# Kernel tuning notes

Measured on AMD Instinct MI355X. Metric: run time of the kernel, lower is better.

The kernel has to match this reference:

```python
import jax, jax.numpy as jnp
import numpy as np

HIDDEN = 16  # hk.LSTM(16)


def lstm_scan(x, W, b, reverse):
    """Haiku LSTM unroll. x: [B,T,D]; W: [D+H, 4H]; b: [4H]. Returns [B,T,H]."""
    B = x.shape[0]

    def step(carry, xt):
        h, c = carry
        gated = jnp.concatenate([xt, h], axis=-1) @ W + b
        i, g, f, o = jnp.split(gated, 4, axis=-1)
        f = jax.nn.sigmoid(f + 1.0)  # haiku forget-gate bias of +1
        c = f * c + jax.nn.sigmoid(i) * jnp.tanh(g)
        h = jax.nn.sigmoid(o) * jnp.tanh(c)
        return (h, c), h

    init = (jnp.zeros((B, HIDDEN), x.dtype), jnp.zeros((B, HIDDEN), x.dtype))
    xt = jnp.swapaxes(x, 0, 1)  # [T,B,D] time-major for scan
    _, outs = jax.lax.scan(step, init, xt, reverse=reverse)
    return jnp.swapaxes(outs, 0, 1)  # [B,T,H]


def setup_inputs() -> dict:
    key = jax.random.key(0)
    ks = jax.random.split(key, 8)
    B, T, D = 4096, 256, 20
    E, H, M, OUT = 64, HIDDEN, 16, 2

    def glorot(k, shape):
        fan_in = shape[0]
        return (jax.random.normal(k, shape, jnp.float32) / np.sqrt(fan_in)).astype(jnp.float32)

    return {
        "x": jax.random.normal(ks[0], (B, T, D), jnp.float32),
        "W0": glorot(ks[1], (D, E)), "b0": jnp.zeros((E,), jnp.float32),
        "Wf": glorot(ks[2], (E + H, 4 * H)), "bf": jnp.zeros((4 * H,), jnp.float32),
        "Wb": glorot(ks[3], (E + H, 4 * H)), "bb": jnp.zeros((4 * H,), jnp.float32),
        "W1": glorot(ks[4], (2 * H, E)), "b1": jnp.zeros((E,), jnp.float32),
        "W2": glorot(ks[5], (E, M)), "b2": jnp.zeros((M,), jnp.float32),
        "W3": glorot(ks[6], (M, OUT)), "b3": jnp.zeros((OUT,), jnp.float32),
    }


def reference(x, W0, b0, Wf, bf, Wb, bb, W1, b1, W2, b2, W3, b3):
    h = jax.nn.relu(x @ W0 + b0)                 # [B,T,64]
    fwd = lstm_scan(h, Wf, bf, reverse=False)    # [B,T,16]
    bwd = lstm_scan(h, Wb, bb, reverse=True)     # [B,T,16], output[t] uses future state
    outs = jnp.concatenate([fwd, bwd], axis=-1)[:, -1, :]  # take last time step, [B,32]
    outs = jax.nn.relu(outs @ W1 + b1)
    outs = jax.nn.relu(outs @ W2 + b2)
    return outs @ W3 + b3
```

## Files before the change

kernel.cpp:

```cpp
#include <hip/hip_runtime.h>


typedef __attribute__((ext_vector_type(8))) short short8;
typedef __attribute__((ext_vector_type(4))) float floatx4;

union F8 { uint32_t u[4]; short8 v; };
union H2 { uint32_t u; _Float16 h[2]; };
union B8 { uint4 q[2]; uint32_t d[8]; };

#define LDW  66
#define LDW2 68

#define LOG2E 1.44269504088896340736f

__device__ __forceinline__ float tanh_fast(float x) {
    float e = __expf(-2.f * x);
    return __fdividef(2.f, 1.f + e) - 1.f;
}

#define ROT(v, S) __int_as_float(__builtin_amdgcn_mov_dpp(__float_as_int(v), 0x120 | (S), 0xf, 0xf, false))

__device__ __forceinline__ void split_pack(const float* f, uint32_t* hi, uint32_t* lo) {
#pragma unroll
    for (int i = 0; i < 4; ++i) {
        uint32_t u0 = __float_as_uint(f[2 * i]), u1 = __float_as_uint(f[2 * i + 1]);
        hi[i] = __builtin_amdgcn_perm(u1, u0, 0x07060302u);
        float r0 = f[2 * i]     - __uint_as_float(u0 & 0xFFFF0000u);
        float r1 = f[2 * i + 1] - __uint_as_float(u1 & 0xFFFF0000u);
        lo[i] = __builtin_amdgcn_perm(__float_as_uint(r1), __float_as_uint(r0), 0x07060302u);
    }
}

__global__ __launch_bounds__(256, 2)
void gpre_gemm(const float* __restrict__ x,
               const float* __restrict__ W0, const float* __restrict__ b0,
               const float* __restrict__ Wf, const float* __restrict__ bf,
               uint32_t* __restrict__ gph)
{
    __shared__ __align__(16) float tA[4][16 * LDW2];
    __shared__ __align__(16) float tB[4][16 * LDW2];

    const int tid  = threadIdx.x;
    const int wv   = tid >> 6;
    const int j    = tid & 63;
    const int nl   = j & 15;
    const int quad = j >> 4;

    F8 B1h[4], B1l[4];
#pragma unroll
    for (int T = 0; T < 4; ++T) {
        float w[8];
#pragma unroll
        for (int e = 0; e < 8; ++e) {
            int k = quad * 8 + e;
            w[e] = (k < 20) ? W0[k * 64 + T * 16 + nl] : 0.f;
        }
        split_pack(w, B1h[T].u, B1l[T].u);
    }
    F8 B2h[4][2], B2l[4][2];
#pragma unroll
    for (int T = 0; T < 4; ++T) {
        const float sgT = (T == 1) ? (-2.f * LOG2E) : (-LOG2E);
#pragma unroll
        for (int KH = 0; KH < 2; ++KH) {
            float w[8];
#pragma unroll
            for (int e = 0; e < 8; ++e) {
                int k = KH * 32 + quad * 8 + e;
                w[e] = Wf[k * 64 + T * 16 + nl] * sgT;
            }
            split_pack(w, B2h[T][KH].u, B2l[T][KH].u);
        }
    }

    float b0v[4], bfv[4];
#pragma unroll
    for (int T = 0; T < 4; ++T) {
        const float sgT = (T == 1) ? (-2.f * LOG2E) : (-LOG2E);
        b0v[T] = b0[T * 16 + nl];
        bfv[T] = (bf[T * 16 + nl] + ((T == 2) ? 1.f : 0.f)) * sgT;
    }

    const size_t base = (size_t)(blockIdx.x * 4 + wv) * 256;

    float4 xp0, xp1;
    {
        const float* xr = x + (base + nl) * 20;
        if (quad < 2) {
            xp0 = *(const float4*)(xr + quad * 8);
            xp1 = *(const float4*)(xr + quad * 8 + 4);
        } else if (quad == 2) {
            xp0 = *(const float4*)(xr + 16);
            xp1 = (float4){0.f, 0.f, 0.f, 0.f};
        } else {
            xp0 = (float4){0.f, 0.f, 0.f, 0.f};
            xp1 = (float4){0.f, 0.f, 0.f, 0.f};
        }
    }

#pragma unroll 1
    for (int tile = 0; tile < 16; ++tile) {
        float xk[8] = {xp0.x, xp0.y, xp0.z, xp0.w, xp1.x, xp1.y, xp1.z, xp1.w};

        {
            int tn = (tile < 15) ? (tile + 1) : 15;
            const float* xr = x + (base + tn * 16 + nl) * 20;
            if (quad < 2) {
                xp0 = *(const float4*)(xr + quad * 8);
                xp1 = *(const float4*)(xr + quad * 8 + 4);
            } else if (quad == 2) {
                xp0 = *(const float4*)(xr + 16);
            }
        }

        F8 A1h, A1l;
        split_pack(xk, A1h.u, A1l.u);

        floatx4 acc1[4];
#pragma unroll
        for (int T = 0; T < 4; ++T) acc1[T] = (floatx4){b0v[T], b0v[T], b0v[T], b0v[T]};
#pragma unroll
        for (int T = 0; T < 4; ++T) {
            acc1[T] = __builtin_amdgcn_mfma_f32_16x16x32_bf16(A1h.v, B1h[T].v, acc1[T], 0, 0, 0);
            acc1[T] = __builtin_amdgcn_mfma_f32_16x16x32_bf16(A1l.v, B1h[T].v, acc1[T], 0, 0, 0);
            acc1[T] = __builtin_amdgcn_mfma_f32_16x16x32_bf16(A1h.v, B1l[T].v, acc1[T], 0, 0, 0);
        }

#pragma unroll
        for (int T = 0; T < 4; ++T)
#pragma unroll
            for (int reg = 0; reg < 4; ++reg)
                tA[wv][(quad * 4 + reg) * LDW2 + T * 16 + nl] = fmaxf(acc1[T][reg], 0.f);
        __builtin_amdgcn_wave_barrier();

        F8 A2h[2], A2l[2];
#pragma unroll
        for (int KH = 0; KH < 2; ++KH) {
            float xe[8];
#pragma unroll
            for (int e = 0; e < 8; ++e)
                xe[e] = tA[wv][nl * LDW2 + KH * 32 + quad * 8 + e];
            split_pack(xe, A2h[KH].u, A2l[KH].u);
        }

        floatx4 acc2[4];
#pragma unroll
        for (int T = 0; T < 4; ++T) acc2[T] = (floatx4){bfv[T], bfv[T], bfv[T], bfv[T]};
#pragma unroll
        for (int T = 0; T < 4; ++T)
#pragma unroll
            for (int KH = 0; KH < 2; ++KH) {
                acc2[T] = __builtin_amdgcn_mfma_f32_16x16x32_bf16(A2h[KH].v, B2h[T][KH].v, acc2[T], 0, 0, 0);
                acc2[T] = __builtin_amdgcn_mfma_f32_16x16x32_bf16(A2l[KH].v, B2h[T][KH].v, acc2[T], 0, 0, 0);
                acc2[T] = __builtin_amdgcn_mfma_f32_16x16x32_bf16(A2h[KH].v, B2l[T][KH].v, acc2[T], 0, 0, 0);
            }

#pragma unroll
        for (int T = 0; T < 4; ++T)
#pragma unroll
            for (int reg = 0; reg < 4; ++reg)
                tB[wv][(quad * 4 + reg) * LDW2 + T * 16 + nl] = acc2[T][reg];
        __builtin_amdgcn_wave_barrier();

        {
            B8 r;
#pragma unroll
            for (int tp = 0; tp < 8; ++tp) {
                float a0 = tB[wv][(2 * tp) * LDW2 + j];
                float a1 = tB[wv][(2 * tp + 1) * LDW2 + j];
                H2 pk;
                pk.h[0] = (_Float16)a0;
                pk.h[1] = (_Float16)a1;
                r.d[tp] = pk.u;
            }
            uint32_t* gp = gph + ((size_t)(blockIdx.x * 4 + wv) * 16 + tile) * 512 + j * 8;
            *(uint4*)(gp)     = r.q[0];
            *(uint4*)(gp + 4) = r.q[1];
        }
        __builtin_amdgcn_wave_barrier();
    }
}

__global__ __launch_bounds__(256, 4)
void lstm_scan(const uint32_t* __restrict__ gph,
               const float* __restrict__ x,
               const float* __restrict__ W0, const float* __restrict__ b0,
               const float* __restrict__ Wf,
               const float* __restrict__ Wb, const float* __restrict__ bb,
               const float* __restrict__ W1, const float* __restrict__ b1,
               const float* __restrict__ W2, const float* __restrict__ b2,
               const float* __restrict__ W3, const float* __restrict__ b3,
               float* __restrict__ out)
{
    __shared__ __align__(16) float xh_sh[4][64];
    __shared__ __align__(16) float h_sh[4][48];

    const int wv   = threadIdx.x >> 6;
    const int j    = threadIdx.x & 63;
    const int b    = blockIdx.x * 4 + wv;
    const int nl   = j & 15;
    const int quad = j >> 4;

    int rot1 = __builtin_amdgcn_mov_dpp(j, 0x121, 0xf, 0xf, false);
    const bool plus = ((rot1 & 15) == ((nl + 1) & 15));

    const float sj = (quad == 1) ? (-2.f * LOG2E) : (-LOG2E);
    float wfhp[16];
#pragma unroll
    for (int s = 0; s < 16; ++s) {
        const int srcq = plus ? ((nl + s) & 15) : ((nl + 16 - s) & 15);
        wfhp[s] = Wf[(64 + srcq) * 64 + j] * sj;
    }

    const float amul = (quad == 1) ? (-4.f * LOG2E) : 1.f;
    const float aadd = (quad == 1) ? ( 2.f * LOG2E) : 0.f;

    const float gmulE = (quad == 1) ? -2.f : -1.f;
    const float amulE = (quad == 1) ? 2.f : 1.f;
    const float aaddE = (quad == 1) ? -1.f : 0.f;

    const int adr_i = 4 * nl;
    const int adr_g = 4 * nl + 64;
    const int adr_f = 4 * nl + 128;
    const int adr_o = 4 * nl + 192;

    float C = 0.f, hh = 0.f;
    const uint32_t* gb = gph + (size_t)b * 8192;

#define STEPG(G)                                                               \
    {                                                                          \
        float v0 = (G), v1;                                                    \
        asm volatile(                                                          \
            "v_fmac_f32 %0, %2, %3\n\t"                                        \
            "s_nop 1\n\t"                                                      \
            "v_mul_f32_dpp %1, %2, %4 row_ror:1 row_mask:0xf bank_mask:0xf\n\t"  \
            "v_fmac_f32_dpp %0, %2, %5 row_ror:2 row_mask:0xf bank_mask:0xf\n\t" \
            "v_fmac_f32_dpp %1, %2, %6 row_ror:3 row_mask:0xf bank_mask:0xf\n\t" \
            "v_fmac_f32_dpp %0, %2, %7 row_ror:4 row_mask:0xf bank_mask:0xf\n\t" \
            "v_fmac_f32_dpp %1, %2, %8 row_ror:5 row_mask:0xf bank_mask:0xf\n\t" \
            "v_fmac_f32_dpp %0, %2, %9 row_ror:6 row_mask:0xf bank_mask:0xf\n\t" \
            "v_fmac_f32_dpp %1, %2, %10 row_ror:7 row_mask:0xf bank_mask:0xf\n\t" \
            "v_fmac_f32_dpp %0, %2, %11 row_ror:8 row_mask:0xf bank_mask:0xf\n\t" \
            "v_fmac_f32_dpp %1, %2, %12 row_ror:9 row_mask:0xf bank_mask:0xf\n\t" \
            "v_fmac_f32_dpp %0, %2, %13 row_ror:10 row_mask:0xf bank_mask:0xf\n\t" \
            "v_fmac_f32_dpp %1, %2, %14 row_ror:11 row_mask:0xf bank_mask:0xf\n\t" \
            "v_fmac_f32_dpp %0, %2, %15 row_ror:12 row_mask:0xf bank_mask:0xf\n\t" \
            "v_fmac_f32_dpp %1, %2, %16 row_ror:13 row_mask:0xf bank_mask:0xf\n\t" \
            "v_fmac_f32_dpp %0, %2, %17 row_ror:14 row_mask:0xf bank_mask:0xf\n\t" \
            "v_fmac_f32_dpp %1, %2, %18 row_ror:15 row_mask:0xf bank_mask:0xf"   \
            : "+&v"(v0), "=&v"(v1)                                             \
            : "v"(hh),                                                         \
              "v"(wfhp[0]),  "v"(wfhp[1]),  "v"(wfhp[2]),  "v"(wfhp[3]),       \
              "v"(wfhp[4]),  "v"(wfhp[5]),  "v"(wfhp[6]),  "v"(wfhp[7]),       \
              "v"(wfhp[8]),  "v"(wfhp[9]),  "v"(wfhp[10]), "v"(wfhp[11]),      \
              "v"(wfhp[12]), "v"(wfhp[13]), "v"(wfhp[14]), "v"(wfhp[15]));     \
        float e = __builtin_amdgcn_exp2f(v0 + v1);                             \
        float y = __builtin_amdgcn_rcpf(1.f + e);                              \
        float a = fmaf(y, amul, aadd);                                         \
        int ab = __float_as_int(a);                                            \
        float ai = __int_as_float(__builtin_amdgcn_ds_bpermute(adr_i, ab));    \
        float ag = __int_as_float(__builtin_amdgcn_ds_bpermute(adr_g, ab));    \
        float af = __int_as_float(__builtin_amdgcn_ds_bpermute(adr_f, ab));    \
        float ao = __int_as_float(__builtin_amdgcn_ds_bpermute(adr_o, ab));    \
        C = fmaf(af, C, ai * ag);                                              \
        float e2 = __builtin_amdgcn_exp2f(C);                                  \
        float th = fmaf(__builtin_amdgcn_rcpf(1.f + e2), 2.f, -1.f);           \
        hh = ao * th;                                                          \
    }

    B8 bufA, bufB;
    bufA.q[0] = *(const uint4*)(gb + j * 8);
    bufA.q[1] = *(const uint4*)(gb + j * 8 + 4);
    bufB.q[0] = *(const uint4*)(gb + 512 + j * 8);
    bufB.q[1] = *(const uint4*)(gb + 512 + j * 8 + 4);

#pragma unroll 1
    for (int blk = 0; blk < 16; blk += 2) {
#pragma unroll
        for (int p = 0; p < 8; ++p) {
            H2 u; u.u = bufA.d[p];
            float g0 = (float)u.h[0];
            float g1 = (float)u.h[1];
            STEPG(g0)
            STEPG(g1)
        }
        {
            int nb = blk + 2; nb = (nb > 15) ? 15 : nb;
            bufA.q[0] = *(const uint4*)(gb + nb * 512 + j * 8);
            bufA.q[1] = *(const uint4*)(gb + nb * 512 + j * 8 + 4);
        }
#pragma unroll
        for (int p = 0; p < 8; ++p) {
            H2 u; u.u = bufB.d[p];
            float g0 = (float)u.h[0];
            float g1 = (float)u.h[1];
            STEPG(g0)
            STEPG(g1)
        }
        {
            int nb = blk + 3; nb = (nb > 15) ? 15 : nb;
            bufB.q[0] = *(const uint4*)(gb + nb * 512 + j * 8);
            bufB.q[1] = *(const uint4*)(gb + nb * 512 + j * 8 + 4);
        }
    }
#undef STEPG

    {
        const float* xr = x + (size_t)b * (256 * 20) + 255 * 20;
        float s = b0[j];
#pragma unroll
        for (int k = 0; k < 20; ++k) s = fmaf(xr[k], W0[k * 64 + j], s);
        xh_sh[wv][j] = fmaxf(s, 0.f);
        if (j < 16) h_sh[wv][j] = hh;
    }
    __builtin_amdgcn_wave_barrier();

    {
        float u0 = bb[j], u1 = 0.f, u2 = 0.f, u3 = 0.f;
        const float* xr = xh_sh[wv];
#pragma unroll
        for (int k4 = 0; k4 < 16; ++k4) {
            u0 = fmaf(xr[4 * k4 + 0], Wb[(4 * k4 + 0) * 64 + j], u0);
            u1 = fmaf(xr[4 * k4 + 1], Wb[(4 * k4 + 1) * 64 + j], u1);
            u2 = fmaf(xr[4 * k4 + 2], Wb[(4 * k4 + 2) * 64 + j], u2);
            u3 = fmaf(xr[4 * k4 + 3], Wb[(4 * k4 + 3) * 64 + j], u3);
        }
        float gated = (u0 + u1) + (u2 + u3);
        float e = __expf(gmulE * gated);
        float y = __fdividef(1.f, 1.f + e);
        float a = fmaf(y, amulE, aaddE);
        float ai = __shfl(a, nl, 64);
        float ag = __shfl(a, nl + 16, 64);
        float ao = __shfl(a, nl + 48, 64);
        float cb = ai * ag;
        float hb = ao * tanh_fast(cb);
        __builtin_amdgcn_wave_barrier();
        if (j < 16) h_sh[wv][16 + j] = hb;
        __builtin_amdgcn_wave_barrier();
    }

    {
        float u0 = b1[j], u1 = 0.f, u2 = 0.f, u3 = 0.f;
        const float4* hs = (const float4*)h_sh[wv];
#pragma unroll
        for (int k4 = 0; k4 < 8; ++k4) {
            float4 v = hs[k4];
            u0 = fmaf(v.x, W1[(4 * k4 + 0) * 64 + j], u0);
            u1 = fmaf(v.y, W1[(4 * k4 + 1) * 64 + j], u1);
            u2 = fmaf(v.z, W1[(4 * k4 + 2) * 64 + j], u2);
            u3 = fmaf(v.w, W1[(4 * k4 + 3) * 64 + j], u3);
        }
        float l1 = fmaxf((u0 + u1) + (u2 + u3), 0.f);
        __builtin_amdgcn_wave_barrier();
        xh_sh[wv][j] = l1;
        __builtin_amdgcn_wave_barrier();

        if (j < 16) {
            float v0 = b2[j], v1 = 0.f, v2 = 0.f, v3 = 0.f;
            const float4* ls = (const float4*)xh_sh[wv];
#pragma unroll
            for (int k4 = 0; k4 < 16; ++k4) {
                float4 v = ls[k4];
                v0 = fmaf(v.x, W2[(4 * k4 + 0) * 16 + j], v0);
                v1 = fmaf(v.y, W2[(4 * k4 + 1) * 16 + j], v1);
                v2 = fmaf(v.z, W2[(4 * k4 + 2) * 16 + j], v2);
                v3 = fmaf(v.w, W2[(4 * k4 + 3) * 16 + j], v3);
            }
            h_sh[wv][32 + j] = fmaxf((v0 + v1) + (v2 + v3), 0.f);
        }
        __builtin_amdgcn_wave_barrier();

        if (j < 2) {
            float o = b3[j];
#pragma unroll
            for (int k = 0; k < 16; ++k)
                o = fmaf(h_sh[wv][32 + k], W3[k * 2 + j], o);
            out[b * 2 + j] = o;
        }
    }
}

__global__ __launch_bounds__(64, 2)
void bilstm_fused_r4(const float* __restrict__ x,
                     const float* __restrict__ W0, const float* __restrict__ b0,
                     const float* __restrict__ Wf, const float* __restrict__ bf,
                     const float* __restrict__ Wb, const float* __restrict__ bb,
                     const float* __restrict__ W1, const float* __restrict__ b1,
                     const float* __restrict__ W2, const float* __restrict__ b2,
                     const float* __restrict__ W3, const float* __restrict__ b3,
                     float* __restrict__ out)
{
    __shared__ __align__(16) float lds_xh[16 * LDW];
    __shared__ __align__(16) float lds_g [16 * LDW];
    __shared__ __align__(16) float h_sh[48];

    const int j    = threadIdx.x;
    const int b    = blockIdx.x;
    const int nl   = j & 15;
    const int quad = j >> 4;

    int rot1 = __builtin_amdgcn_mov_dpp(j, 0x121, 0xf, 0xf, false);
    const bool plus = ((rot1 & 15) == ((nl + 1) & 15));

    float wfhp[16];
#pragma unroll
    for (int s = 0; s < 16; ++s) {
        const int srcq = plus ? ((nl + s) & 15) : ((nl + 16 - s) & 15);
        wfhp[s] = Wf[(64 + srcq) * 64 + j];
    }

    F8 B1h[4], B1l[4];
#pragma unroll
    for (int T = 0; T < 4; ++T) {
        float w[8];
#pragma unroll
        for (int e = 0; e < 8; ++e) {
            int k = quad * 8 + e;
            w[e] = (k < 20) ? W0[k * 64 + T * 16 + nl] : 0.f;
        }
        split_pack(w, B1h[T].u, B1l[T].u);
    }
    F8 B2h[4][2], B2l[4][2];
#pragma unroll
    for (int T = 0; T < 4; ++T)
#pragma unroll
        for (int KH = 0; KH < 2; ++KH) {
            float w[8];
#pragma unroll
            for (int e = 0; e < 8; ++e) {
                int k = KH * 32 + quad * 8 + e;
                w[e] = Wf[k * 64 + T * 16 + nl];
            }
            split_pack(w, B2h[T][KH].u, B2l[T][KH].u);
        }

    float b0v[4], bfv[4];
#pragma unroll
    for (int T = 0; T < 4; ++T) {
        b0v[T] = b0[T * 16 + nl];
        bfv[T] = bf[T * 16 + nl];
    }

    const float gmul  = (quad == 1) ? -2.f : -1.f;
    const float gbias = (quad == 2) ? 1.f : 0.f;
    const float amul  = (quad == 1) ? 2.f : 1.f;
    const float aadd  = (quad == 1) ? -1.f : 0.f;
    const bool  b0sel = (quad & 1) != 0;
    const bool  b1sel = (quad & 2) != 0;

    float c = 0.f, hh = 0.f;
    const float* xb = x + (size_t)b * (256 * 20);

#pragma unroll 1
    for (int ch = 0; ch < 16; ++ch) {
        const int t0 = ch * 16;
        const float* xrow = xb + (size_t)(t0 + nl) * 20;
        float xk[8];
#pragma unroll
        for (int e = 0; e < 8; ++e) {
            int k = quad * 8 + e;
            xk[e] = (k < 20) ? xrow[k] : 0.f;
        }
        F8 A1h, A1l;
        split_pack(xk, A1h.u, A1l.u);

        floatx4 acc1[4];
#pragma unroll
        for (int T = 0; T < 4; ++T) acc1[T] = (floatx4){b0v[T], b0v[T], b0v[T], b0v[T]};
#pragma unroll
        for (int T = 0; T < 4; ++T) {
            acc1[T] = __builtin_amdgcn_mfma_f32_16x16x32_bf16(A1h.v, B1h[T].v, acc1[T], 0, 0, 0);
            acc1[T] = __builtin_amdgcn_mfma_f32_16x16x32_bf16(A1l.v, B1h[T].v, acc1[T], 0, 0, 0);
            acc1[T] = __builtin_amdgcn_mfma_f32_16x16x32_bf16(A1h.v, B1l[T].v, acc1[T], 0, 0, 0);
        }
#pragma unroll
        for (int T = 0; T < 4; ++T)
#pragma unroll
            for (int reg = 0; reg < 4; ++reg)
                lds_xh[(quad * 4 + reg) * LDW + T * 16 + nl] = fmaxf(acc1[T][reg], 0.f);
        __builtin_amdgcn_wave_barrier();

        F8 A2h[2], A2l[2];
#pragma unroll
        for (int KH = 0; KH < 2; ++KH) {
            float xe[8];
#pragma unroll
            for (int e = 0; e < 8; ++e)
                xe[e] = lds_xh[nl * LDW + KH * 32 + quad * 8 + e];
            split_pack(xe, A2h[KH].u, A2l[KH].u);
        }

        floatx4 acc2[4];
#pragma unroll
        for (int T = 0; T < 4; ++T) acc2[T] = (floatx4){bfv[T], bfv[T], bfv[T], bfv[T]};
#pragma unroll
        for (int T = 0; T < 4; ++T)
#pragma unroll
            for (int KH = 0; KH < 2; ++KH) {
                acc2[T] = __builtin_amdgcn_mfma_f32_16x16x32_bf16(A2h[KH].v, B2h[T][KH].v, acc2[T], 0, 0, 0);
                acc2[T] = __builtin_amdgcn_mfma_f32_16x16x32_bf16(A2l[KH].v, B2h[T][KH].v, acc2[T], 0, 0, 0);
                acc2[T] = __builtin_amdgcn_mfma_f32_16x16x32_bf16(A2h[KH].v, B2l[T][KH].v, acc2[T], 0, 0, 0);
            }
#pragma unroll
        for (int T = 0; T < 4; ++T)
#pragma unroll
            for (int reg = 0; reg < 4; ++reg)
                lds_g[(quad * 4 + reg) * LDW + T * 16 + nl] = acc2[T][reg];
        __builtin_amdgcn_wave_barrier();

        float gcur = lds_g[j];
#pragma unroll
        for (int tau = 0; tau < 16; ++tau) {
            float gnext = lds_g[((tau < 15) ? (tau + 1) : 15) * LDW + j];
            float v0 = hh * wfhp[0];
            float v1 = ROT(hh, 1) * wfhp[1];
            float v2 = ROT(hh, 2) * wfhp[2];
            float v3 = ROT(hh, 3) * wfhp[3];
            v0 = fmaf(ROT(hh, 4),  wfhp[4],  v0);
            v1 = fmaf(ROT(hh, 5),  wfhp[5],  v1);
            v2 = fmaf(ROT(hh, 6),  wfhp[6],  v2);
            v3 = fmaf(ROT(hh, 7),  wfhp[7],  v3);
            v0 = fmaf(ROT(hh, 8),  wfhp[8],  v0);
            v1 = fmaf(ROT(hh, 9),  wfhp[9],  v1);
            v2 = fmaf(ROT(hh, 10), wfhp[10], v2);
            v3 = fmaf(ROT(hh, 11), wfhp[11], v3);
            v0 = fmaf(ROT(hh, 12), wfhp[12], v0);
            v1 = fmaf(ROT(hh, 13), wfhp[13], v1);
            v2 = fmaf(ROT(hh, 14), wfhp[14], v2);
            v3 = fmaf(ROT(hh, 15), wfhp[15], v3);
            float gated = gcur + ((v0 + v1) + (v2 + v3));

            float e = __expf(gmul * (gated + gbias));
            float y = __fdividef(1.f, 1.f + e);
            float a = fmaf(y, amul, aadd);

            float d1 = __shfl_xor(a, 16);
            float d2 = __shfl_xor(a, 32);
            float d3 = __shfl_xor(a, 48);
            float lo  = b0sel ? d1 : a;
            float hi  = b0sel ? d3 : d2;
            float lo1 = b0sel ? a  : d1;
            float hi1 = b0sel ? d2 : d3;
            float ai = b1sel ? hi  : lo;
            float ag = b1sel ? hi1 : lo1;
            float af = b1sel ? lo  : hi;
            float ao = b1sel ? lo1 : hi1;

            c  = fmaf(af, c, ai * ag);
            hh = ao * tanh_fast(c);
            gcur = gnext;
        }
    }

    if (j < 16) h_sh[j] = hh;
    __builtin_amdgcn_wave_barrier();

    {
        float u0 = bb[j], u1 = 0.f, u2 = 0.f, u3 = 0.f;
        const float* xr = &lds_xh[15 * LDW];
#pragma unroll
        for (int k4 = 0; k4 < 16; ++k4) {
            u0 = fmaf(xr[4 * k4 + 0], Wb[(4 * k4 + 0) * 64 + j], u0);
            u1 = fmaf(xr[4 * k4 + 1], Wb[(4 * k4 + 1) * 64 + j], u1);
            u2 = fmaf(xr[4 * k4 + 2], Wb[(4 * k4 + 2) * 64 + j], u2);
            u3 = fmaf(xr[4 * k4 + 3], Wb[(4 * k4 + 3) * 64 + j], u3);
        }
        float gated = (u0 + u1) + (u2 + u3);
        float e = __expf(gmul * gated);
        float y = __fdividef(1.f, 1.f + e);
        float a = fmaf(y, amul, aadd);
        float ai = __shfl(a, nl, 64);
        float ag = __shfl(a, nl + 16, 64);
        float ao = __shfl(a, nl + 48, 64);
        float cb = ai * ag;
        float hb = ao * tanh_fast(cb);
        __builtin_amdgcn_wave_barrier();
        if (j < 16) h_sh[16 + j] = hb;
        __builtin_amdgcn_wave_barrier();
    }

    {
        float u0 = b1[j], u1 = 0.f, u2 = 0.f, u3 = 0.f;
        const float4* hs = (const float4*)h_sh;
#pragma unroll
        for (int k4 = 0; k4 < 8; ++k4) {
            float4 v = hs[k4];
            u0 = fmaf(v.x, W1[(4 * k4 + 0) * 64 + j], u0);
            u1 = fmaf(v.y, W1[(4 * k4 + 1) * 64 + j], u1);
            u2 = fmaf(v.z, W1[(4 * k4 + 2) * 64 + j], u2);
            u3 = fmaf(v.w, W1[(4 * k4 + 3) * 64 + j], u3);
        }
        float l1 = fmaxf((u0 + u1) + (u2 + u3), 0.f);
        __builtin_amdgcn_wave_barrier();
        lds_g[j] = l1;
        __builtin_amdgcn_wave_barrier();

        if (j < 16) {
            float v0 = b2[j], v1 = 0.f, v2 = 0.f, v3 = 0.f;
            const float4* ls = (const float4*)lds_g;
#pragma unroll
            for (int k4 = 0; k4 < 16; ++k4) {
                float4 v = ls[k4];
                v0 = fmaf(v.x, W2[(4 * k4 + 0) * 16 + j], v0);
                v1 = fmaf(v.y, W2[(4 * k4 + 1) * 16 + j], v1);
                v2 = fmaf(v.z, W2[(4 * k4 + 2) * 16 + j], v2);
                v3 = fmaf(v.w, W2[(4 * k4 + 3) * 16 + j], v3);
            }
            h_sh[32 + j] = fmaxf((v0 + v1) + (v2 + v3), 0.f);
        }
        __builtin_amdgcn_wave_barrier();

        if (j < 2) {
            float o = b3[j];
#pragma unroll
            for (int k = 0; k < 16; ++k)
                o = fmaf(h_sh[32 + k], W3[k * 2 + j], o);
            out[b * 2 + j] = o;
        }
    }
}

extern "C" void kernel_launch(void* const* d_in, const int* in_sizes, int n_in,
                              void* d_out, int out_size, void* d_ws, size_t ws_size,
                              hipStream_t stream) {
    const float* x  = (const float*)d_in[0];
    const float* W0 = (const float*)d_in[1];
    const float* b0 = (const float*)d_in[2];
    const float* Wf = (const float*)d_in[3];
    const float* bf = (const float*)d_in[4];
    const float* Wb = (const float*)d_in[5];
    const float* bb = (const float*)d_in[6];
    const float* W1 = (const float*)d_in[7];
    const float* b1 = (const float*)d_in[8];
    const float* W2 = (const float*)d_in[9];
    const float* b2 = (const float*)d_in[10];
    const float* W3 = (const float*)d_in[11];
    const float* b3 = (const float*)d_in[12];
    float* outp = (float*)d_out;

    const size_t need = (size_t)4096 * 128 * 64 * sizeof(uint32_t);
    if (ws_size >= need) {
        uint32_t* gph = (uint32_t*)d_ws;
        hipLaunchKernelGGL(gpre_gemm, dim3(1024), dim3(256), 0, stream,
                           x, W0, b0, Wf, bf, gph);
        hipLaunchKernelGGL(lstm_scan, dim3(1024), dim3(256), 0, stream,
                           gph, x, W0, b0, Wf, Wb, bb, W1, b1, W2, b2, W3, b3, outp);
    } else {
        hipLaunchKernelGGL(bilstm_fused_r4, dim3(4096), dim3(64), 0, stream,
                           x, W0, b0, Wf, bf, Wb, bb, W1, b1, W2, b2, W3, b3, outp);
    }
}
```

Baseline: 255.6 us.

## Interleave two batch rows per wave in LSTM scan to hide latency

Each wave now runs the recurrent scan for two independent batch rows at once, interleaving their DPP matvecs, transcendental ops and bpermute gathers so that one chain's latency overlaps the other's. The grid is halved to 512 blocks to match. This exposes instruction-level parallelism in a latency-bound serial recurrence. In exchange it raises register pressure from the doubled buffers and state, and halves the number of waves, which can reduce occupancy and latency hiding across waves.

```diff
diff --git a/kernel.cpp b/kernel.cpp
--- a/kernel.cpp
+++ b/kernel.cpp
@@ -197,7 +197,7 @@
 
     const int wv   = threadIdx.x >> 6;
     const int j    = threadIdx.x & 63;
-    const int b    = blockIdx.x * 4 + wv;
+    const int bA   = (blockIdx.x * 4 + wv) * 2;
     const int nl   = j & 15;
     const int quad = j >> 4;
 
@@ -224,12 +224,12 @@
     const int adr_f = 4 * nl + 128;
     const int adr_o = 4 * nl + 192;
 
-    float C = 0.f, hh = 0.f;
-    const uint32_t* gb = gph + (size_t)b * 8192;
-
-#define STEPG(G)                                                               \
-    {                                                                          \
-        float v0 = (G), v1;                                                    \
+    float CA = 0.f, hhA = 0.f;
+    float CB = 0.f, hhB = 0.f;
+    const uint32_t* gbA = gph + (size_t)bA * 8192;
+    const uint32_t* gbB = gbA + 8192;
+
+#define MATVEC(V0, V1, HH)                                                     \
         asm volatile(                                                          \
             "v_fmac_f32 %0, %2, %3\n\t"                                        \
             "s_nop 1\n\t"                                                      \
@@ -248,135 +248,172 @@
             "v_fmac_f32_dpp %1, %2, %16 row_ror:13 row_mask:0xf bank_mask:0xf\n\t" \
             "v_fmac_f32_dpp %0, %2, %17 row_ror:14 row_mask:0xf bank_mask:0xf\n\t" \
             "v_fmac_f32_dpp %1, %2, %18 row_ror:15 row_mask:0xf bank_mask:0xf"   \
-            : "+&v"(v0), "=&v"(v1)                                             \
-            : "v"(hh),                                                         \
+            : "+&v"(V0), "=&v"(V1)                                             \
+            : "v"(HH),                                                         \
               "v"(wfhp[0]),  "v"(wfhp[1]),  "v"(wfhp[2]),  "v"(wfhp[3]),       \
               "v"(wfhp[4]),  "v"(wfhp[5]),  "v"(wfhp[6]),  "v"(wfhp[7]),       \
               "v"(wfhp[8]),  "v"(wfhp[9]),  "v"(wfhp[10]), "v"(wfhp[11]),      \
-              "v"(wfhp[12]), "v"(wfhp[13]), "v"(wfhp[14]), "v"(wfhp[15]));     \
-        float e = __builtin_amdgcn_exp2f(v0 + v1);                             \
-        float y = __builtin_amdgcn_rcpf(1.f + e);                              \
-        float a = fmaf(y, amul, aadd);                                         \
-        int ab = __float_as_int(a);                                            \
-        float ai = __int_as_float(__builtin_amdgcn_ds_bpermute(adr_i, ab));    \
-        float ag = __int_as_float(__builtin_amdgcn_ds_bpermute(adr_g, ab));    \
-        float af = __int_as_float(__builtin_amdgcn_ds_bpermute(adr_f, ab));    \
-        float ao = __int_as_float(__builtin_amdgcn_ds_bpermute(adr_o, ab));    \
-        C = fmaf(af, C, ai * ag);                                              \
-        float e2 = __builtin_amdgcn_exp2f(C);                                  \
-        float th = fmaf(__builtin_amdgcn_rcpf(1.f + e2), 2.f, -1.f);           \
-        hh = ao * th;                                                          \
-    }
-
-    B8 bufA, bufB;
-    bufA.q[0] = *(const uint4*)(gb + j * 8);
-    bufA.q[1] = *(const uint4*)(gb + j * 8 + 4);
-    bufB.q[0] = *(const uint4*)(gb + 512 + j * 8);
-    bufB.q[1] = *(const uint4*)(gb + 512 + j * 8 + 4);
+              "v"(wfhp[12]), "v"(wfhp[13]), "v"(wfhp[14]), "v"(wfhp[15]))
+
+#define STEP2(GA, GB)                                                          \
+    {                                                                          \
+        float vA0 = (GA), vA1;                                                 \
+        float vB0 = (GB), vB1;                                                 \
+        MATVEC(vA0, vA1, hhA);                                                 \
+        MATVEC(vB0, vB1, hhB);                                                 \
+        float eA = __builtin_amdgcn_exp2f(vA0 + vA1);                          \
+        float eB = __builtin_amdgcn_exp2f(vB0 + vB1);                          \
+        float yA = __builtin_amdgcn_rcpf(1.f + eA);                            \
+        float yB = __builtin_amdgcn_rcpf(1.f + eB);                            \
+        float aA = fmaf(yA, amul, aadd);                                       \
+        float aB = fmaf(yB, amul, aadd);                                       \
+        int abA = __float_as_int(aA);                                          \
+        int abB = __float_as_int(aB);                                          \
+        float aiA = __int_as_float(__builtin_amdgcn_ds_bpermute(adr_i, abA));  \
+        float agA = __int_as_float(__builtin_amdgcn_ds_bpermute(adr_g, abA));  \
+        float afA = __int_as_float(__builtin_amdgcn_ds_bpermute(adr_f, abA));  \
+        float aoA = __int_as_float(__builtin_amdgcn_ds_bpermute(adr_o, abA));  \
+        float aiB = __int_as_float(__builtin_amdgcn_ds_bpermute(adr_i, abB));  \
+        float agB = __int_as_float(__builtin_amdgcn_ds_bpermute(adr_g, abB));  \
+        float afB = __int_as_float(__builtin_amdgcn_ds_bpermute(adr_f, abB));  \
+        float aoB = __int_as_float(__builtin_amdgcn_ds_bpermute(adr_o, abB));  \
+        CA = fmaf(afA, CA, aiA * agA);                                         \
+        CB = fmaf(afB, CB, aiB * agB);                                         \
+        float e2A = __builtin_amdgcn_exp2f(CA);                                \
+        float e2B = __builtin_amdgcn_exp2f(CB);                                \
+        float thA = fmaf(__builtin_amdgcn_rcpf(1.f + e2A), 2.f, -1.f);         \
+        float thB = fmaf(__builtin_amdgcn_rcpf(1.f + e2B), 2.f, -1.f);         \
+        hhA = aoA * thA;                                                       \
+        hhB = aoB * thB;                                                       \
+    }
+
+    B8 bufA0, bufA1, bufB0, bufB1;
+    bufA0.q[0] = *(const uint4*)(gbA + j * 8);
+    bufA0.q[1] = *(const uint4*)(gbA + j * 8 + 4);
+    bufA1.q[0] = *(const uint4*)(gbA + 512 + j * 8);
+    bufA1.q[1] = *(const uint4*)(gbA + 512 + j * 8 + 4);
+    bufB0.q[0] = *(const uint4*)(gbB + j * 8);
+    bufB0.q[1] = *(const uint4*)(gbB + j * 8 + 4);
+    bufB1.q[0] = *(const uint4*)(gbB + 512 + j * 8);
+    bufB1.q[1] = *(const uint4*)(gbB + 512 + j * 8 + 4);
 
 #pragma unroll 1
     for (int blk = 0; blk < 16; blk += 2) {
 #pragma unroll
         for (int p = 0; p < 8; ++p) {
-            H2 u; u.u = bufA.d[p];
-            float g0 = (float)u.h[0];
-            float g1 = (float)u.h[1];
-            STEPG(g0)
-            STEPG(g1)
+            H2 uA; uA.u = bufA0.d[p];
+            H2 uB; uB.u = bufB0.d[p];
+            float gA0 = (float)uA.h[0], gA1 = (float)uA.h[1];
+            float gB0 = (float)uB.h[0], gB1 = (float)uB.h[1];
+            STEP2(gA0, gB0)
+            STEP2(gA1, gB1)
         }
         {
             int nb = blk + 2; nb = (nb > 15) ? 15 : nb;
-            bufA.q[0] = *(const uint4*)(gb + nb * 512 + j * 8);
-            bufA.q[1] = *(const uint4*)(gb + nb * 512 + j * 8 + 4);
+            bufA0.q[0] = *(const uint4*)(gbA + nb * 512 + j * 8);
+            bufA0.q[1] = *(const uint4*)(gbA + nb * 512 + j * 8 + 4);
+            bufB0.q[0] = *(const uint4*)(gbB + nb * 512 + j * 8);
+            bufB0.q[1] = *(const uint4*)(gbB + nb * 512 + j * 8 + 4);
         }
 #pragma unroll
         for (int p = 0; p < 8; ++p) {
-            H2 u; u.u = bufB.d[p];
-            float g0 = (float)u.h[0];
-            float g1 = (float)u.h[1];
-            STEPG(g0)
-            STEPG(g1)
+            H2 uA; uA.u = bufA1.d[p];
+            H2 uB; uB.u = bufB1.d[p];
+            float gA0 = (float)uA.h[0], gA1 = (float)uA.h[1];
+            float gB0 = (float)uB.h[0], gB1 = (float)uB.h[1];
+            STEP2(gA0, gB0)
+            STEP2(gA1, gB1)
         }
         {
             int nb = blk + 3; nb = (nb > 15) ? 15 : nb;
-            bufB.q[0] = *(const uint4*)(gb + nb * 512 + j * 8);
-            bufB.q[1] = *(const uint4*)(gb + nb * 512 + j * 8 + 4);
-        }
-    }
-#undef STEPG
-
-    {
-        const float* xr = x + (size_t)b * (256 * 20) + 255 * 20;
-        float s = b0[j];
-#pragma unroll
-        for (int k = 0; k < 20; ++k) s = fmaf(xr[k], W0[k * 64 + j], s);
-        xh_sh[wv][j] = fmaxf(s, 0.f);
-        if (j < 16) h_sh[wv][j] = hh;
-    }
-    __builtin_amdgcn_wave_barrier();
-
-    {
-        float u0 = bb[j], u1 = 0.f, u2 = 0.f, u3 = 0.f;
-        const float* xr = xh_sh[wv];
-#pragma unroll
-        for (int k4 = 0; k4 < 16; ++k4) {
-            u0 = fmaf(xr[4 * k4 + 0], Wb[(4 * k4 + 0) * 64 + j], u0);
-            u1 = fmaf(xr[4 * k4 + 1], Wb[(4 * k4 + 1) * 64 + j], u1);
-            u2 = fmaf(xr[4 * k4 + 2], Wb[(4 * k4 + 2) * 64 + j], u2);
-            u3 = fmaf(xr[4 * k4 + 3], Wb[(4 * k4 + 3) * 64 + j], u3);
-        }
-        float gated = (u0 + u1) + (u2 + u3);
-        float e = __expf(gmulE * gated);
-        float y = __fdividef(1.f, 1.f + e);
-        float a = fmaf(y, amulE, aaddE);
-        float ai = __shfl(a, nl, 64);
-        float ag = __shfl(a, nl + 16, 64);
-        float ao = __shfl(a, nl + 48, 64);
-        float cb = ai * ag;
-        float hb = ao * tanh_fast(cb);
-        __builtin_amdgcn_wave_barrier();
-        if (j < 16) h_sh[wv][16 + j] = hb;
-        __builtin_amdgcn_wave_barrier();
-    }
-
-    {
-        float u0 = b1[j], u1 = 0.f, u2 = 0.f, u3 = 0.f;
-        const float4* hs = (const float4*)h_sh[wv];
-#pragma unroll
-        for (int k4 = 0; k4 < 8; ++k4) {
-            float4 v = hs[k4];
-            u0 = fmaf(v.x, W1[(4 * k4 + 0) * 64 + j], u0);
-            u1 = fmaf(v.y, W1[(4 * k4 + 1) * 64 + j], u1);
-            u2 = fmaf(v.z, W1[(4 * k4 + 2) * 64 + j], u2);
-            u3 = fmaf(v.w, W1[(4 * k4 + 3) * 64 + j], u3);
-        }
-        float l1 = fmaxf((u0 + u1) + (u2 + u3), 0.f);
-        __builtin_amdgcn_wave_barrier();
-        xh_sh[wv][j] = l1;
-        __builtin_amdgcn_wave_barrier();
-
-        if (j < 16) {
-            float v0 = b2[j], v1 = 0.f, v2 = 0.f, v3 = 0.f;
-            const float4* ls = (const float4*)xh_sh[wv];
+            bufA1.q[0] = *(const uint4*)(gbA + nb * 512 + j * 8);
+            bufA1.q[1] = *(const uint4*)(gbA + nb * 512 + j * 8 + 4);
+            bufB1.q[0] = *(const uint4*)(gbB + nb * 512 + j * 8);
+            bufB1.q[1] = *(const uint4*)(gbB + nb * 512 + j * 8 + 4);
+        }
+    }
+#undef STEP2
+#undef MATVEC
+
+#pragma unroll 1
+    for (int bi = 0; bi < 2; ++bi) {
+        const int b   = bA + bi;
+        const float hhx = (bi == 0) ? hhA : hhB;
+
+        {
+            const float* xr = x + (size_t)b * (256 * 20) + 255 * 20;
+            float s = b0[j];
+#pragma unroll
+            for (int k = 0; k < 20; ++k) s = fmaf(xr[k], W0[k * 64 + j], s);
+            xh_sh[wv][j] = fmaxf(s, 0.f);
+            if (j < 16) h_sh[wv][j] = hhx;
+        }
+        __builtin_amdgcn_wave_barrier();
+
+        {
+            float u0 = bb[j], u1 = 0.f, u2 = 0.f, u3 = 0.f;
+            const float* xr = xh_sh[wv];
 #pragma unroll
             for (int k4 = 0; k4 < 16; ++k4) {
-                float4 v = ls[k4];
-                v0 = fmaf(v.x, W2[(4 * k4 + 0) * 16 + j], v0);
-                v1 = fmaf(v.y, W2[(4 * k4 + 1) * 16 + j], v1);
-                v2 = fmaf(v.z, W2[(4 * k4 + 2) * 16 + j], v2);
-                v3 = fmaf(v.w, W2[(4 * k4 + 3) * 16 + j], v3);
-            }
-            h_sh[wv][32 + j] = fmaxf((v0 + v1) + (v2 + v3), 0.f);
-        }
-        __builtin_amdgcn_wave_barrier();
-
-        if (j < 2) {
-            float o = b3[j];
-#pragma unroll
-            for (int k = 0; k < 16; ++k)
-                o = fmaf(h_sh[wv][32 + k], W3[k * 2 + j], o);
-            out[b * 2 + j] = o;
-        }
+                u0 = fmaf(xr[4 * k4 + 0], Wb[(4 * k4 + 0) * 64 + j], u0);
+                u1 = fmaf(xr[4 * k4 + 1], Wb[(4 * k4 + 1) * 64 + j], u1);
+                u2 = fmaf(xr[4 * k4 + 2], Wb[(4 * k4 + 2) * 64 + j], u2);
+                u3 = fmaf(xr[4 * k4 + 3], Wb[(4 * k4 + 3) * 64 + j], u3);
+            }
+            float gated = (u0 + u1) + (u2 + u3);
+            float e = __expf(gmulE * gated);
+            float y = __fdividef(1.f, 1.f + e);
+            float a = fmaf(y, amulE, aaddE);
+            float ai = __shfl(a, nl, 64);
+            float ag = __shfl(a, nl + 16, 64);
+            float ao = __shfl(a, nl + 48, 64);
+            float cb = ai * ag;
+            float hb = ao * tanh_fast(cb);
+            __builtin_amdgcn_wave_barrier();
+            if (j < 16) h_sh[wv][16 + j] = hb;
+            __builtin_amdgcn_wave_barrier();
+        }
+
+        {
+            float u0 = b1[j], u1 = 0.f, u2 = 0.f, u3 = 0.f;
+            const float4* hs = (const float4*)h_sh[wv];
+#pragma unroll
+            for (int k4 = 0; k4 < 8; ++k4) {
+                float4 v = hs[k4];
+                u0 = fmaf(v.x, W1[(4 * k4 + 0) * 64 + j], u0);
+                u1 = fmaf(v.y, W1[(4 * k4 + 1) * 64 + j], u1);
+                u2 = fmaf(v.z, W1[(4 * k4 + 2) * 64 + j], u2);
+                u3 = fmaf(v.w, W1[(4 * k4 + 3) * 64 + j], u3);
+            }
+            float l1 = fmaxf((u0 + u1) + (u2 + u3), 0.f);
+            __builtin_amdgcn_wave_barrier();
+            xh_sh[wv][j] = l1;
+            __builtin_amdgcn_wave_barrier();
+
+            if (j < 16) {
+                float v0 = b2[j], v1 = 0.f, v2 = 0.f, v3 = 0.f;
+                const float4* ls = (const float4*)xh_sh[wv];
+#pragma unroll
+                for (int k4 = 0; k4 < 16; ++k4) {
+                    float4 v = ls[k4];
+                    v0 = fmaf(v.x, W2[(4 * k4 + 0) * 16 + j], v0);
+                    v1 = fmaf(v.y, W2[(4 * k4 + 1) * 16 + j], v1);
+                    v2 = fmaf(v.z, W2[(4 * k4 + 2) * 16 + j], v2);
+                    v3 = fmaf(v.w, W2[(4 * k4 + 3) * 16 + j], v3);
+                }
+                h_sh[wv][32 + j] = fmaxf((v0 + v1) + (v2 + v3), 0.f);
+            }
+            __builtin_amdgcn_wave_barrier();
+
+            if (j < 2) {
+                float o = b3[j];
+#pragma unroll
+                for (int k = 0; k < 16; ++k)
+                    o = fmaf(h_sh[wv][32 + k], W3[k * 2 + j], o);
+                out[b * 2 + j] = o;
+            }
+        }
+        __builtin_amdgcn_wave_barrier();
     }
 }
 
@@ -643,7 +680,7 @@
         uint32_t* gph = (uint32_t*)d_ws;
         hipLaunchKernelGGL(gpre_gemm, dim3(1024), dim3(256), 0, stream,
                            x, W0, b0, Wf, bf, gph);
-        hipLaunchKernelGGL(lstm_scan, dim3(1024), dim3(256), 0, stream,
+        hipLaunchKernelGGL(lstm_scan, dim3(512), dim3(256), 0, stream,
                            gph, x, W0, b0, Wf, Wb, bb, W1, b1, W2, b2, W3, b3, outp);
     } else {
         hipLaunchKernelGGL(bilstm_fused_r4, dim3(4096), dim3(64), 0, stream,
```

After: 280.9 us. 9.9% more time.
